# Performance work log

Hardware: AMD Instinct MI355X
Metric: run time of the kernel (lower is better)

Reference implementation:

```python
import jax, jax.numpy as jnp
import numpy as np

B, T, C = 2, 4096, 768
H = 12
HD = C // H  # 64

def setup_inputs() -> dict:
    key = jax.random.key(0)
    k1, k2, k3 = jax.random.split(key, 3)
    scale_in = 1.0 / np.sqrt(C)
    return {
        "x": jax.random.normal(k1, (B, T, C), dtype=jnp.float32),
        "w_qkv": jax.random.normal(k2, (C, 3 * C), dtype=jnp.float32) * scale_in,
        "b_qkv": jnp.zeros((3 * C,), dtype=jnp.float32),
        "w_proj": jax.random.normal(k3, (C, C), dtype=jnp.float32) * scale_in,
        "b_proj": jnp.zeros((C,), dtype=jnp.float32),
    }

def reference(x, w_qkv, b_qkv, w_proj, b_proj):
    # Dropout in eval mode (identity), matching module.eval().
    Bx, Tx, Cx = x.shape
    qkv = x @ w_qkv + b_qkv                      # [B,T,3C]
    q, k, v = jnp.split(qkv, 3, axis=-1)
    def to_heads(t):
        return t.reshape(Bx, Tx, H, HD).transpose(0, 2, 1, 3)  # [B,H,T,hd]
    q, k, v = to_heads(q), to_heads(k), to_heads(v)
    att = jnp.einsum('bhqd,bhkd->bhqk', q, k) / jnp.sqrt(jnp.float32(HD))
    causal = jnp.tril(jnp.ones((Tx, Tx), dtype=bool))
    att = jnp.where(causal[None, None], att, -jnp.inf)
    att = jax.nn.softmax(att, axis=-1)
    y = jnp.einsum('bhqk,bhkd->bhqd', att, v)    # [B,H,T,hd]
    y = y.transpose(0, 2, 1, 3).reshape(Bx, Tx, Cx)
    return y @ w_proj + b_proj
```

## Files before the change

### kernel.cpp

```cpp
#include <hip/hip_runtime.h>


#define TSEQ 4096
#define NH 12
#define CDIM 768

typedef __bf16 bf16;
typedef __attribute__((ext_vector_type(8))) __bf16 bf16x8;
typedef __attribute__((ext_vector_type(4))) __bf16 bf16x4;
typedef __attribute__((ext_vector_type(4))) float f32x4;

__device__ __forceinline__ void gload16(const void* g, void* l) {
  __builtin_amdgcn_global_load_lds(
      (const __attribute__((address_space(1))) void*)g,
      (__attribute__((address_space(3))) void*)l, 16, 0, 0);
}

__device__ __forceinline__ float fexp2(float x) {
  return __builtin_amdgcn_exp2f(x);
}

__global__ void convert_x_kernel(const float* __restrict__ x,
                                 bf16* __restrict__ xb, int n) {
  int i = (blockIdx.x * blockDim.x + threadIdx.x) * 4;
  if (i < n) {
    float4 v = *(const float4*)(x + i);
    bf16x4 o;
    o[0] = (bf16)v.x; o[1] = (bf16)v.y; o[2] = (bf16)v.z; o[3] = (bf16)v.w;
    *(bf16x4*)(xb + i) = o;
  }
}

__global__ void transpose_w_kernel(const float* __restrict__ src,
                                   bf16* __restrict__ dst, int R, int Cc) {
  __shared__ float tile[32][33];
  int tx = threadIdx.x, ty = threadIdx.y;
  int c0 = blockIdx.x * 32, r0 = blockIdx.y * 32;
#pragma unroll
  for (int i = 0; i < 4; ++i)
    tile[ty + i * 8][tx] = src[(size_t)(r0 + ty + i * 8) * Cc + c0 + tx];
  __syncthreads();
#pragma unroll
  for (int i = 0; i < 4; ++i)
    dst[(size_t)(c0 + ty + i * 8) * R + r0 + tx] = (bf16)tile[tx][ty + i * 8];
}

template <int MODE>
__global__ __launch_bounds__(256) void gemm_kernel(
    const bf16* __restrict__ A, const bf16* __restrict__ BT,
    const float* __restrict__ bias, bf16* __restrict__ qk_out,
    bf16* __restrict__ vT_out, float* __restrict__ c_out) {
  constexpr int K = 768;
  __shared__ alignas(16) bf16 As[128 * 64];
  __shared__ alignas(16) bf16 Bs[128 * 64];
  const int t = threadIdx.x;
  const int l = t & 63, w = t >> 6;
  const int l15 = l & 15, lg = l >> 4;
  const int nwg = gridDim.x * gridDim.y;
  int id = blockIdx.y * gridDim.x + blockIdx.x;
  id = (id & 7) * (nwg >> 3) + (id >> 3);
  const int m0 = (id / gridDim.x) << 7, n0 = (id % gridDim.x) << 7;
  const int wr = w >> 1, wc = w & 1;

  f32x4 acc[4][4] = {};

  const int r0 = t >> 3;
  const int kb8 = (((t & 7) ^ (r0 & 7)) << 3);
  const bf16* Asrc = A + (size_t)(m0 + r0) * K + kb8;
  const bf16* Bsrc = BT + (size_t)(n0 + r0) * K + kb8;

  for (int kt = 0; kt < K / 64; ++kt) {
#pragma unroll
    for (int i = 0; i < 4; ++i)
      gload16(Asrc + kt * 64 + (size_t)i * 32 * K, (char*)As + w * 1024 + i * 4096);
#pragma unroll
    for (int i = 0; i < 4; ++i)
      gload16(Bsrc + kt * 64 + (size_t)i * 32 * K, (char*)Bs + w * 1024 + i * 4096);
    __syncthreads();
#pragma unroll
    for (int kk = 0; kk < 2; ++kk) {
      bf16x8 af[4], bfv[4];
#pragma unroll
      for (int m = 0; m < 4; ++m) {
        int r = (wr << 6) + (m << 4) + l15;
        int kb = (kk << 2) + lg;
        af[m] = *(const bf16x8*)((const char*)As + r * 128 + ((kb ^ (r & 7)) << 4));
      }
#pragma unroll
      for (int n = 0; n < 4; ++n) {
        int r = (wc << 6) + (n << 4) + l15;
        int kb = (kk << 2) + lg;
        bfv[n] = *(const bf16x8*)((const char*)Bs + r * 128 + ((kb ^ (r & 7)) << 4));
      }
#pragma unroll
      for (int m = 0; m < 4; ++m)
#pragma unroll
        for (int n = 0; n < 4; ++n)
          acc[m][n] = __builtin_amdgcn_mfma_f32_16x16x32_bf16(af[m], bfv[n],
                                                              acc[m][n], 0, 0, 0);
    }
    __syncthreads();
  }

#pragma unroll
  for (int m = 0; m < 4; ++m) {
    int row = m0 + (wr << 6) + (m << 4) + (lg << 2);
    int b = row >> 12, tt = row & 4095;
#pragma unroll
    for (int n = 0; n < 4; ++n) {
      int col = n0 + (wc << 6) + (n << 4) + l15;
      float bv = bias[col];
      if (MODE == 0) {
        if (col < 1536) {
          float sc = (col < 768) ? 0.18033688011112042f : 1.0f;
          bf16* dst = qk_out + (size_t)(b * TSEQ + tt) * 1536 + col;
#pragma unroll
          for (int j = 0; j < 4; ++j)
            dst[(size_t)j * 1536] = (bf16)((acc[m][n][j] + bv) * sc);
        } else {
          int nl = col - 1536;
          bf16* dst = vT_out +
              ((size_t)(b * NH + (nl >> 6)) * 64 + (nl & 63)) * TSEQ + tt;
#pragma unroll
          for (int j = 0; j < 4; ++j) dst[j] = (bf16)(acc[m][n][j] + bv);
        }
      } else {
        float* dst = c_out + (size_t)row * 768 + col;
#pragma unroll
        for (int j = 0; j < 4; ++j) dst[(size_t)j * 768] = acc[m][n][j] + bv;
      }
    }
  }
}

__global__ __launch_bounds__(256) void attn_kernel(
    const bf16* __restrict__ qk,
    const bf16* __restrict__ vT,
    bf16* __restrict__ y) {
  __shared__ alignas(16) char lds[40960];
  const int t = threadIdx.x;
  const int l = t & 63, w = t >> 6;
  const int l15 = l & 15, lg = l >> 4;
  const int nwg = gridDim.x * gridDim.y;
  int id = blockIdx.y * gridDim.x + blockIdx.x;
  id = (id & 7) * (nwg >> 3) + (id >> 3);
  const int p = id & 31, bh = id >> 5;
  const int b = bh / NH, h = bh % NH;
  const bf16* qbase = qk + (size_t)b * TSEQ * 1536 + h * 64;
  const bf16* kbase = qbase + 768;
  const bf16* vbase = vT + (size_t)bh * 64 * TSEQ;

  const int r0 = t >> 3;
  const int kb8 = (((t & 7) ^ (r0 & 7)) << 3);

  int bufp = 0;
  {
    const int q0 = (63 - p) << 6;
#pragma unroll
    for (int i = 0; i < 2; ++i) {
      gload16(qbase + (size_t)(q0 + i * 32 + r0) * 1536 + kb8,
              lds + w * 1024 + i * 4096);
      gload16(kbase + (size_t)(i * 32 + r0) * 1536 + kb8,
              lds + 8192 + w * 1024 + i * 4096);
      gload16(vbase + (size_t)(i * 32 + r0) * TSEQ + kb8,
              lds + 16384 + w * 1024 + i * 4096);
    }
  }
  __syncthreads();

  for (int pass = 0; pass < 2; ++pass) {
    const int qb = pass ? p : 63 - p;
    const int q0 = qb << 6;
    const int nkt = qb + 1;
    const int qw = q0 + (w << 4);

    bf16x8 qf[2];
#pragma unroll
    for (int kk = 0; kk < 2; ++kk) {
      int r = (w << 4) + l15;
      int kb = (kk << 2) + lg;
      qf[kk] = *(const bf16x8*)(lds + r * 128 + ((kb ^ (r & 7)) << 4));
    }

    f32x4 o[4] = {};
    float mrun = -__builtin_inff();
    float lrun = 0.f;

    for (int kt = 0; kt < nkt; ++kt) {
      const int kv0 = kt << 6;
      const char* kvb = lds + 8192 + (bufp << 14);

      if (kt + 1 < nkt) {
        const int kv1 = (kt + 1) << 6;
        char* nb = lds + 8192 + ((bufp ^ 1) << 14);
#pragma unroll
        for (int i = 0; i < 2; ++i) {
          gload16(kbase + (size_t)(kv1 + i * 32 + r0) * 1536 + kb8,
                  nb + w * 1024 + i * 4096);
          gload16(vbase + (size_t)(i * 32 + r0) * TSEQ + kv1 + kb8,
                  nb + 8192 + w * 1024 + i * 4096);
        }
      } else if (pass == 0) {
        char* nb = lds + 8192 + ((bufp ^ 1) << 14);
#pragma unroll
        for (int i = 0; i < 2; ++i) {
          gload16(kbase + (size_t)(i * 32 + r0) * 1536 + kb8,
                  nb + w * 1024 + i * 4096);
          gload16(vbase + (size_t)(i * 32 + r0) * TSEQ + kb8,
                  nb + 8192 + w * 1024 + i * 4096);
        }
      }

      f32x4 s[4] = {};
#pragma unroll
      for (int kk = 0; kk < 2; ++kk) {
        bf16x8 kf[4];
#pragma unroll
        for (int m = 0; m < 4; ++m) {
          int r = (m << 4) + l15;
          int kb = (kk << 2) + lg;
          kf[m] = *(const bf16x8*)(kvb + r * 128 + ((kb ^ (r & 7)) << 4));
        }
#pragma unroll
        for (int m = 0; m < 4; ++m)
          s[m] = __builtin_amdgcn_mfma_f32_16x16x32_bf16(kf[m], qf[kk],
                                                         s[m], 0, 0, 0);
      }
      if (kv0 + 63 > qw) {
        int q = qw + l15;
#pragma unroll
        for (int m = 0; m < 4; ++m) {
          int kvr = kv0 + (m << 4) + (lg << 2);
#pragma unroll
          for (int j = 0; j < 4; ++j)
            if (kvr + j > q) s[m][j] = -__builtin_inff();
        }
      }
      float cmax = -__builtin_inff();
#pragma unroll
      for (int m = 0; m < 4; ++m)
#pragma unroll
        for (int j = 0; j < 4; ++j) cmax = fmaxf(cmax, s[m][j]);
      cmax = fmaxf(cmax, __shfl_xor(cmax, 16));
      cmax = fmaxf(cmax, __shfl_xor(cmax, 32));
      if (__any(cmax > mrun + 8.f)) {
        float mnew = fmaxf(mrun, cmax);
        float alpha = fexp2(mrun - mnew);
        mrun = mnew;
        lrun *= alpha;
#pragma unroll
        for (int j = 0; j < 4; ++j) {
          int rr = (lg << 2) + j;
          float a = __shfl(alpha, (l & 48) | rr);
#pragma unroll
          for (int no = 0; no < 4; ++no) o[no][j] *= a;
        }
      }
      float ps = 0.f;
#pragma unroll
      for (int m = 0; m < 4; ++m)
#pragma unroll
        for (int j = 0; j < 4; ++j) {
          float pv = fexp2(s[m][j] - mrun);
          s[m][j] = pv;
          ps += pv;
        }
      ps += __shfl_xor(ps, 16);
      ps += __shfl_xor(ps, 32);
      lrun += ps;
      {
        int q = l15;
        char* pbase = lds + w * 2048 + q * 128;
        int sw = (q & 7) << 4;
#pragma unroll
        for (int m = 0; m < 4; ++m) {
          bf16x4 pv;
#pragma unroll
          for (int j = 0; j < 4; ++j) pv[j] = (bf16)s[m][j];
          *(bf16x4*)(pbase + (((m << 5) + (lg << 3)) ^ sw)) = pv;
        }
      }
#pragma unroll
      for (int kk = 0; kk < 2; ++kk) {
        int kb = (kk << 2) + lg;
        int q = l15;
        bf16x8 pa = *(const bf16x8*)(lds + w * 2048 + q * 128 + ((kb ^ (q & 7)) << 4));
        bf16x8 vb[4];
#pragma unroll
        for (int no = 0; no < 4; ++no) {
          int d = (no << 4) + l15;
          vb[no] = *(const bf16x8*)(kvb + 8192 + d * 128 + ((kb ^ (d & 7)) << 4));
        }
#pragma unroll
        for (int no = 0; no < 4; ++no)
          o[no] = __builtin_amdgcn_mfma_f32_16x16x32_bf16(pa, vb[no],
                                                          o[no], 0, 0, 0);
      }
      __syncthreads();
      bufp ^= 1;
    }

#pragma unroll
    for (int j = 0; j < 4; ++j) {
      int rr = (lg << 2) + j;
      float lv = __shfl(lrun, (l & 48) | rr);
      float linv = 1.0f / lv;
      int qrow = qw + rr;
      size_t base = ((size_t)(b * TSEQ + qrow)) * 768 + h * 64;
#pragma unroll
      for (int no = 0; no < 4; ++no)
        y[base + (no << 4) + l15] = (bf16)(o[no][j] * linv);
    }

    if (pass == 0) {
      const int q0n = p << 6;
#pragma unroll
      for (int i = 0; i < 2; ++i)
        gload16(qbase + (size_t)(q0n + i * 32 + r0) * 1536 + kb8,
                lds + w * 1024 + i * 4096);
      __syncthreads();
    }
  }
}

extern "C" void kernel_launch(void* const* d_in, const int* in_sizes, int n_in,
                              void* d_out, int out_size, void* d_ws,
                              size_t ws_size, hipStream_t stream) {
  const float* x = (const float*)d_in[0];
  const float* w_qkv = (const float*)d_in[1];
  const float* b_qkv = (const float*)d_in[2];
  const float* w_proj = (const float*)d_in[3];
  const float* b_proj = (const float*)d_in[4];
  float* out = (float*)d_out;
  char* ws = (char*)d_ws;

  bf16* xb     = (bf16*)(ws);
  bf16* wqkvT  = (bf16*)(ws + 12582912);
  bf16* wprojT = (bf16*)(ws + 16121856);
  bf16* qkbuf  = (bf16*)(ws + 17301504);
  bf16* vTbuf  = (bf16*)(ws + 42467328);
  bf16* ybuf   = (bf16*)(ws + 55050240);

  convert_x_kernel<<<6144, 256, 0, stream>>>(x, xb, 2 * TSEQ * CDIM);
  transpose_w_kernel<<<dim3(72, 24), dim3(32, 8), 0, stream>>>(w_qkv, wqkvT, 768, 2304);
  transpose_w_kernel<<<dim3(24, 24), dim3(32, 8), 0, stream>>>(w_proj, wprojT, 768, 768);
  gemm_kernel<0><<<dim3(18, 64), 256, 0, stream>>>(xb, wqkvT, b_qkv, qkbuf, vTbuf, nullptr);
  attn_kernel<<<dim3(32, 24), 256, 0, stream>>>(qkbuf, vTbuf, ybuf);
  gemm_kernel<1><<<dim3(6, 64), 256, 0, stream>>>(ybuf, wprojT, b_proj, nullptr, nullptr, out);
}
```

Measured before the change: 258.2 us.

## Give each attention workgroup one query block and add MFMA priority hints

The attention kernel used to pair a long and a short causal query block in each workgroup (two passes) to balance work. It now launches twice as many workgroups, one per query block, ordered longest-first, and drops the pass loop and the cross-pass prefetch. It also wraps the MFMA sections in s_setprio to favour matrix issue over other waves. This adds more parallelism and simpler control flow but gives up the static load balancing, so the finish depends on the hardware scheduler handling uneven block lengths.

```diff
diff --git a/kernel.cpp b/kernel.cpp
--- a/kernel.cpp
+++ b/kernel.cpp
@@ -144,7 +144,8 @@
   const int nwg = gridDim.x * gridDim.y;
   int id = blockIdx.y * gridDim.x + blockIdx.x;
   id = (id & 7) * (nwg >> 3) + (id >> 3);
-  const int p = id & 31, bh = id >> 5;
+  const int qb = 63 - (id & 63);
+  const int bh = id >> 6;
   const int b = bh / NH, h = bh % NH;
   const bf16* qbase = qk + (size_t)b * TSEQ * 1536 + h * 64;
   const bf16* kbase = qbase + 768;
@@ -152,174 +153,153 @@
 
   const int r0 = t >> 3;
   const int kb8 = (((t & 7) ^ (r0 & 7)) << 3);
-
+  const int q0 = qb << 6;
+  const int nkt = qb + 1;
+  const int qw = q0 + (w << 4);
+
+#pragma unroll
+  for (int i = 0; i < 2; ++i) {
+    gload16(qbase + (size_t)(q0 + i * 32 + r0) * 1536 + kb8,
+            lds + w * 1024 + i * 4096);
+    gload16(kbase + (size_t)(i * 32 + r0) * 1536 + kb8,
+            lds + 8192 + w * 1024 + i * 4096);
+    gload16(vbase + (size_t)(i * 32 + r0) * TSEQ + kb8,
+            lds + 16384 + w * 1024 + i * 4096);
+  }
+  __syncthreads();
+
+  bf16x8 qf[2];
+#pragma unroll
+  for (int kk = 0; kk < 2; ++kk) {
+    int r = (w << 4) + l15;
+    int kb = (kk << 2) + lg;
+    qf[kk] = *(const bf16x8*)(lds + r * 128 + ((kb ^ (r & 7)) << 4));
+  }
+
+  f32x4 o[4] = {};
+  float mrun = -__builtin_inff();
+  float lrun = 0.f;
   int bufp = 0;
-  {
-    const int q0 = (63 - p) << 6;
-#pragma unroll
-    for (int i = 0; i < 2; ++i) {
-      gload16(qbase + (size_t)(q0 + i * 32 + r0) * 1536 + kb8,
-              lds + w * 1024 + i * 4096);
-      gload16(kbase + (size_t)(i * 32 + r0) * 1536 + kb8,
-              lds + 8192 + w * 1024 + i * 4096);
-      gload16(vbase + (size_t)(i * 32 + r0) * TSEQ + kb8,
-              lds + 16384 + w * 1024 + i * 4096);
-    }
-  }
-  __syncthreads();
-
-  for (int pass = 0; pass < 2; ++pass) {
-    const int qb = pass ? p : 63 - p;
-    const int q0 = qb << 6;
-    const int nkt = qb + 1;
-    const int qw = q0 + (w << 4);
-
-    bf16x8 qf[2];
+
+  for (int kt = 0; kt < nkt; ++kt) {
+    const int kv0 = kt << 6;
+    const char* kvb = lds + 8192 + (bufp << 14);
+
+    if (kt + 1 < nkt) {
+      const int kv1 = (kt + 1) << 6;
+      char* nb = lds + 8192 + ((bufp ^ 1) << 14);
+#pragma unroll
+      for (int i = 0; i < 2; ++i) {
+        gload16(kbase + (size_t)(kv1 + i * 32 + r0) * 1536 + kb8,
+                nb + w * 1024 + i * 4096);
+        gload16(vbase + (size_t)(i * 32 + r0) * TSEQ + kv1 + kb8,
+                nb + 8192 + w * 1024 + i * 4096);
+      }
+    }
+
+    f32x4 s[4] = {};
+    __builtin_amdgcn_s_setprio(1);
 #pragma unroll
     for (int kk = 0; kk < 2; ++kk) {
-      int r = (w << 4) + l15;
+      bf16x8 kf[4];
+#pragma unroll
+      for (int m = 0; m < 4; ++m) {
+        int r = (m << 4) + l15;
+        int kb = (kk << 2) + lg;
+        kf[m] = *(const bf16x8*)(kvb + r * 128 + ((kb ^ (r & 7)) << 4));
+      }
+#pragma unroll
+      for (int m = 0; m < 4; ++m)
+        s[m] = __builtin_amdgcn_mfma_f32_16x16x32_bf16(kf[m], qf[kk],
+                                                       s[m], 0, 0, 0);
+    }
+    __builtin_amdgcn_s_setprio(0);
+    if (kv0 + 63 > qw) {
+      int q = qw + l15;
+#pragma unroll
+      for (int m = 0; m < 4; ++m) {
+        int kvr = kv0 + (m << 4) + (lg << 2);
+#pragma unroll
+        for (int j = 0; j < 4; ++j)
+          if (kvr + j > q) s[m][j] = -__builtin_inff();
+      }
+    }
+    float cmax = -__builtin_inff();
+#pragma unroll
+    for (int m = 0; m < 4; ++m)
+#pragma unroll
+      for (int j = 0; j < 4; ++j) cmax = fmaxf(cmax, s[m][j]);
+    cmax = fmaxf(cmax, __shfl_xor(cmax, 16));
+    cmax = fmaxf(cmax, __shfl_xor(cmax, 32));
+    if (__any(cmax > mrun + 8.f)) {
+      float mnew = fmaxf(mrun, cmax);
+      float alpha = fexp2(mrun - mnew);
+      mrun = mnew;
+      lrun *= alpha;
+#pragma unroll
+      for (int j = 0; j < 4; ++j) {
+        int rr = (lg << 2) + j;
+        float a = __shfl(alpha, (l & 48) | rr);
+#pragma unroll
+        for (int no = 0; no < 4; ++no) o[no][j] *= a;
+      }
+    }
+    float ps = 0.f;
+#pragma unroll
+    for (int m = 0; m < 4; ++m)
+#pragma unroll
+      for (int j = 0; j < 4; ++j) {
+        float pv = fexp2(s[m][j] - mrun);
+        s[m][j] = pv;
+        ps += pv;
+      }
+    ps += __shfl_xor(ps, 16);
+    ps += __shfl_xor(ps, 32);
+    lrun += ps;
+    {
+      int q = l15;
+      char* pbase = lds + w * 2048 + q * 128;
+      int sw = (q & 7) << 4;
+#pragma unroll
+      for (int m = 0; m < 4; ++m) {
+        bf16x4 pv;
+#pragma unroll
+        for (int j = 0; j < 4; ++j) pv[j] = (bf16)s[m][j];
+        *(bf16x4*)(pbase + (((m << 5) + (lg << 3)) ^ sw)) = pv;
+      }
+    }
+    __builtin_amdgcn_s_setprio(1);
+#pragma unroll
+    for (int kk = 0; kk < 2; ++kk) {
       int kb = (kk << 2) + lg;
-      qf[kk] = *(const bf16x8*)(lds + r * 128 + ((kb ^ (r & 7)) << 4));
-    }
-
-    f32x4 o[4] = {};
-    float mrun = -__builtin_inff();
-    float lrun = 0.f;
-
-    for (int kt = 0; kt < nkt; ++kt) {
-      const int kv0 = kt << 6;
-      const char* kvb = lds + 8192 + (bufp << 14);
-
-      if (kt + 1 < nkt) {
-        const int kv1 = (kt + 1) << 6;
-        char* nb = lds + 8192 + ((bufp ^ 1) << 14);
-#pragma unroll
-        for (int i = 0; i < 2; ++i) {
-          gload16(kbase + (size_t)(kv1 + i * 32 + r0) * 1536 + kb8,
-                  nb + w * 1024 + i * 4096);
-          gload16(vbase + (size_t)(i * 32 + r0) * TSEQ + kv1 + kb8,
-                  nb + 8192 + w * 1024 + i * 4096);
-        }
-      } else if (pass == 0) {
-        char* nb = lds + 8192 + ((bufp ^ 1) << 14);
-#pragma unroll
-        for (int i = 0; i < 2; ++i) {
-          gload16(kbase + (size_t)(i * 32 + r0) * 1536 + kb8,
-                  nb + w * 1024 + i * 4096);
-          gload16(vbase + (size_t)(i * 32 + r0) * TSEQ + kb8,
-                  nb + 8192 + w * 1024 + i * 4096);
-        }
-      }
-
-      f32x4 s[4] = {};
-#pragma unroll
-      for (int kk = 0; kk < 2; ++kk) {
-        bf16x8 kf[4];
-#pragma unroll
-        for (int m = 0; m < 4; ++m) {
-          int r = (m << 4) + l15;
-          int kb = (kk << 2) + lg;
-          kf[m] = *(const bf16x8*)(kvb + r * 128 + ((kb ^ (r & 7)) << 4));
-        }
-#pragma unroll
-        for (int m = 0; m < 4; ++m)
-          s[m] = __builtin_amdgcn_mfma_f32_16x16x32_bf16(kf[m], qf[kk],
-                                                         s[m], 0, 0, 0);
-      }
-      if (kv0 + 63 > qw) {
-        int q = qw + l15;
-#pragma unroll
-        for (int m = 0; m < 4; ++m) {
-          int kvr = kv0 + (m << 4) + (lg << 2);
-#pragma unroll
-          for (int j = 0; j < 4; ++j)
-            if (kvr + j > q) s[m][j] = -__builtin_inff();
-        }
-      }
-      float cmax = -__builtin_inff();
-#pragma unroll
-      for (int m = 0; m < 4; ++m)
-#pragma unroll
-        for (int j = 0; j < 4; ++j) cmax = fmaxf(cmax, s[m][j]);
-      cmax = fmaxf(cmax, __shfl_xor(cmax, 16));
-      cmax = fmaxf(cmax, __shfl_xor(cmax, 32));
-      if (__any(cmax > mrun + 8.f)) {
-        float mnew = fmaxf(mrun, cmax);
-        float alpha = fexp2(mrun - mnew);
-        mrun = mnew;
-        lrun *= alpha;
-#pragma unroll
-        for (int j = 0; j < 4; ++j) {
-          int rr = (lg << 2) + j;
-          float a = __shfl(alpha, (l & 48) | rr);
-#pragma unroll
-          for (int no = 0; no < 4; ++no) o[no][j] *= a;
-        }
-      }
-      float ps = 0.f;
-#pragma unroll
-      for (int m = 0; m < 4; ++m)
-#pragma unroll
-        for (int j = 0; j < 4; ++j) {
-          float pv = fexp2(s[m][j] - mrun);
-          s[m][j] = pv;
-          ps += pv;
-        }
-      ps += __shfl_xor(ps, 16);
-      ps += __shfl_xor(ps, 32);
-      lrun += ps;
-      {
-        int q = l15;
-        char* pbase = lds + w * 2048 + q * 128;
-        int sw = (q & 7) << 4;
-#pragma unroll
-        for (int m = 0; m < 4; ++m) {
-          bf16x4 pv;
-#pragma unroll
-          for (int j = 0; j < 4; ++j) pv[j] = (bf16)s[m][j];
-          *(bf16x4*)(pbase + (((m << 5) + (lg << 3)) ^ sw)) = pv;
-        }
-      }
-#pragma unroll
-      for (int kk = 0; kk < 2; ++kk) {
-        int kb = (kk << 2) + lg;
-        int q = l15;
-        bf16x8 pa = *(const bf16x8*)(lds + w * 2048 + q * 128 + ((kb ^ (q & 7)) << 4));
-        bf16x8 vb[4];
-#pragma unroll
-        for (int no = 0; no < 4; ++no) {
-          int d = (no << 4) + l15;
-          vb[no] = *(const bf16x8*)(kvb + 8192 + d * 128 + ((kb ^ (d & 7)) << 4));
-        }
-#pragma unroll
-        for (int no = 0; no < 4; ++no)
-          o[no] = __builtin_amdgcn_mfma_f32_16x16x32_bf16(pa, vb[no],
-                                                          o[no], 0, 0, 0);
-      }
-      __syncthreads();
-      bufp ^= 1;
-    }
-
-#pragma unroll
-    for (int j = 0; j < 4; ++j) {
-      int rr = (lg << 2) + j;
-      float lv = __shfl(lrun, (l & 48) | rr);
-      float linv = 1.0f / lv;
-      int qrow = qw + rr;
-      size_t base = ((size_t)(b * TSEQ + qrow)) * 768 + h * 64;
+      int q = l15;
+      bf16x8 pa = *(const bf16x8*)(lds + w * 2048 + q * 128 + ((kb ^ (q & 7)) << 4));
+      bf16x8 vb[4];
+#pragma unroll
+      for (int no = 0; no < 4; ++no) {
+        int d = (no << 4) + l15;
+        vb[no] = *(const bf16x8*)(kvb + 8192 + d * 128 + ((kb ^ (d & 7)) << 4));
+      }
 #pragma unroll
       for (int no = 0; no < 4; ++no)
-        y[base + (no << 4) + l15] = (bf16)(o[no][j] * linv);
-    }
-
-    if (pass == 0) {
-      const int q0n = p << 6;
-#pragma unroll
-      for (int i = 0; i < 2; ++i)
-        gload16(qbase + (size_t)(q0n + i * 32 + r0) * 1536 + kb8,
-                lds + w * 1024 + i * 4096);
-      __syncthreads();
-    }
+        o[no] = __builtin_amdgcn_mfma_f32_16x16x32_bf16(pa, vb[no],
+                                                        o[no], 0, 0, 0);
+    }
+    __builtin_amdgcn_s_setprio(0);
+    __syncthreads();
+    bufp ^= 1;
+  }
+
+#pragma unroll
+  for (int j = 0; j < 4; ++j) {
+    int rr = (lg << 2) + j;
+    float lv = __shfl(lrun, (l & 48) | rr);
+    float linv = 1.0f / lv;
+    int qrow = qw + rr;
+    size_t base = ((size_t)(b * TSEQ + qrow)) * 768 + h * 64;
+#pragma unroll
+    for (int no = 0; no < 4; ++no)
+      y[base + (no << 4) + l15] = (bf16)(o[no][j] * linv);
   }
 }
 
@@ -345,6 +325,6 @@
   transpose_w_kernel<<<dim3(72, 24), dim3(32, 8), 0, stream>>>(w_qkv, wqkvT, 768, 2304);
   transpose_w_kernel<<<dim3(24, 24), dim3(32, 8), 0, stream>>>(w_proj, wprojT, 768, 768);
   gemm_kernel<0><<<dim3(18, 64), 256, 0, stream>>>(xb, wqkvT, b_qkv, qkbuf, vTbuf, nullptr);
-  attn_kernel<<<dim3(32, 24), 256, 0, stream>>>(qkbuf, vTbuf, ybuf);
+  attn_kernel<<<dim3(64, 24), 256, 0, stream>>>(qkbuf, vTbuf, ybuf);
   gemm_kernel<1><<<dim3(6, 64), 256, 0, stream>>>(ybuf, wprojT, b_proj, nullptr, nullptr, out);
 }
```

After: 257.5 us. No clear change (-0.3%).
